# Performance work log

Hardware: AMD Instinct MI355X
Metric: run time of the kernel (lower is better)

Reference implementation:

```python
import jax, jax.numpy as jnp
import numpy as np
from functools import partial

# norse LIFAdEx default parameters
DT = 0.001
TAU_SYN_INV = 1.0 / 5e-3   # 200.0
TAU_MEM_INV = 1.0 / 1e-2   # 100.0
TAU_ADA_INV = 2.0
ADAPT_CURRENT = 4.0
ADAPT_SPIKE = 0.02
DELTA_T = 0.5
V_LEAK = 0.0
V_TH = 1.0
V_RESET = 0.0
ALPHA = 100.0              # superspike surrogate sharpness
TAU_FILTER_INV = 223.1435511314


@jax.custom_vjp
def superspike(x):
    # forward: heaviside; backward: superspike surrogate grad
    return (x > 0).astype(x.dtype)

def _ss_fwd(x):
    return superspike(x), x

def _ss_bwd(x, g):
    return (g / (ALPHA * jnp.abs(x) + 1.0) ** 2,)

superspike.defvjp(_ss_fwd, _ss_bwd)


def lif_adex_recurrent(x, W_in, W_rec):
    """x: (T,B,F) -> spikes (T,B,H). norse lif_adex_step semantics."""
    T, B, _ = x.shape
    H = W_rec.shape[0]
    # precompute feed-forward input current for all steps: (T,B,H)
    i_in = jnp.einsum('tbf,hf->tbh', x, W_in)

    def step(carry, ic):
        z, v, i, a = carry
        dv = DT * TAU_MEM_INV * ((V_LEAK - v)
                                 + DELTA_T * jnp.exp((v - V_TH) / DELTA_T)
                                 + i - a)
        v_dec = v + dv
        i_dec = i - DT * TAU_SYN_INV * i
        a_dec = a + DT * TAU_ADA_INV * (ADAPT_CURRENT * (v - V_LEAK) - a)
        z_new = superspike(v_dec - V_TH)
        v_new = (1.0 - z_new) * v_dec + z_new * V_RESET
        i_new = i_dec + ic + z @ W_rec.T
        a_new = a_dec + z_new * ADAPT_SPIKE
        return (z_new, v_new, i_new, a_new), z_new

    z0 = jnp.zeros((B, H), x.dtype)
    init = (z0, z0, z0, z0)
    _, spikes = jax.lax.scan(step, init, i_in)
    return spikes


def exp_filter(spikes, W_out, b_out):
    """Linear readout + exponential low-pass filter over time."""
    y = jnp.einsum('tbh,oh->tbo', spikes, W_out) + b_out  # (T,B,O)
    k = DT * TAU_FILTER_INV

    def step(o_prev, y_t):
        o = o_prev + k * (y_t - o_prev)
        return o, o

    o0 = y[0]
    _, rest = jax.lax.scan(step, o0, y[1:])
    return jnp.concatenate([o0[None], rest], axis=0)


def setup_inputs() -> dict:
    key = jax.random.key(0)
    kx, k1, k2, k3, k4 = jax.random.split(key, 5)
    T, B, F, H, O = 500, 128, 128, 512, 32
    x = jax.random.normal(kx, (T, B, F), dtype=jnp.float32)
    W_in = jax.random.normal(k1, (H, F), dtype=jnp.float32) * np.sqrt(2.0 / F)
    W_rec = jax.random.normal(k2, (H, H), dtype=jnp.float32) * np.sqrt(2.0 / H)
    W_out = jax.random.normal(k3, (O, H), dtype=jnp.float32) * np.sqrt(1.0 / H)
    b_out = jax.random.normal(k4, (O,), dtype=jnp.float32) * 0.01
    return {'x': x, 'W_in': W_in, 'W_rec': W_rec, 'W_out': W_out, 'b_out': b_out}


def reference(x, W_in, W_rec, W_out, b_out):
    spikes = lif_adex_recurrent(x, W_in, W_rec)
    return exp_filter(spikes, W_out, b_out)
```

## Files before the change

kernel.cpp:

```cpp
#include <hip/hip_runtime.h>
#include <hip/hip_bf16.h>
#include <cstdint>
#include <cstddef>

#define T_STEPS 500
#define BATCH   128
#define FDIM    128
#define HDIM    512
#define ODIM    32
#define M_ROWS  (T_STEPS * BATCH)
#define ZOFF    (512u << 11)
#define ZOFFB   (512u << 10)

typedef __attribute__((ext_vector_type(8))) __bf16 bf16x8;
typedef __attribute__((ext_vector_type(4))) float  f32x4;

__device__ __forceinline__ float bfbits2f(unsigned short u) {
    union { unsigned int i; float f; } c; c.i = ((unsigned int)u) << 16; return c.f;
}
__device__ __forceinline__ float asf(unsigned int u) {
    union { unsigned int i; float f; } c; c.i = u; return c.f;
}
__device__ __forceinline__ void lds_barrier() {
    asm volatile("s_waitcnt lgkmcnt(0)" ::: "memory");
    __builtin_amdgcn_s_barrier();
}

__global__ void detect_kernel(const unsigned short* __restrict__ xw, int* __restrict__ flag) {
    __shared__ int cnt;
    if (threadIdx.x == 0) cnt = 0;
    __syncthreads();
    unsigned short w = xw[threadIdx.x * 2];
    int e = (w >> 7) & 0xFF;
    if (e >= 170) atomicAdd(&cnt, 1);
    __syncthreads();
    if (threadIdx.x == 0) *flag = (cnt >= 8) ? 1 : 0;
}

__global__ void prep_kernel(const void* __restrict__ Wrec,
                            const void* __restrict__ Wout,
                            const void* __restrict__ bout,
                            const void* __restrict__ Win,
                            const int* __restrict__ flag,
                            float* __restrict__ WrecT,
                            unsigned short* __restrict__ WrecTb,
                            float* __restrict__ WoutT,
                            float* __restrict__ WinT,
                            float* __restrict__ bout32) {
    const int fp32 = *flag;
    int idx = blockIdx.x * blockDim.x + threadIdx.x;
    if (fp32) {
        if (idx < HDIM * HDIM) {
            int h = idx / HDIM, hp = idx % HDIM;
            WrecT[hp * HDIM + h] = ((const float*)Wrec)[idx];
        }
        if (idx < HDIM) WrecT[HDIM * HDIM + idx] = 0.f;
        if (idx < HDIM * FDIM) {
            int h = idx / FDIM, f = idx % FDIM;
            WinT[f * HDIM + h] = ((const float*)Win)[idx];
        }
    } else {
        if (idx < HDIM * HDIM) {
            int h = idx / HDIM, hp = idx % HDIM;
            WrecTb[hp * HDIM + h] = ((const unsigned short*)Wrec)[idx];
        }
        if (idx < HDIM) WrecTb[HDIM * HDIM + idx] = 0;
    }
    if (idx < ODIM * HDIM) {
        int o = idx / HDIM, h = idx % HDIM;
        WoutT[h * ODIM + o] = fp32 ? ((const float*)Wout)[idx]
                                   : bfbits2f(((const unsigned short*)Wout)[idx]);
    }
    if (idx < ODIM)
        bout32[idx] = fp32 ? ((const float*)bout)[idx]
                           : bfbits2f(((const unsigned short*)bout)[idx]);
}

__global__ __launch_bounds__(256) void iin_gemm_mfma(const __hip_bfloat16* __restrict__ x,
                                                     const __hip_bfloat16* __restrict__ Win,
                                                     const int* __restrict__ flag,
                                                     float* __restrict__ iin) {
    if (*flag != 0) return;
    const int mt   = blockIdx.x;
    const int nt   = blockIdx.y;
    const int wave = threadIdx.x >> 6;
    const int lane = threadIdx.x & 63;
    const int l15  = lane & 15;
    const int quad = lane >> 4;
    const int m_base = mt * 64 + wave * 16;
    const int n_base = nt * 64;

    const __bf16* xb = reinterpret_cast<const __bf16*>(x);
    const __bf16* wb = reinterpret_cast<const __bf16*>(Win);

    f32x4 acc[4] = {{0.f,0.f,0.f,0.f},{0.f,0.f,0.f,0.f},{0.f,0.f,0.f,0.f},{0.f,0.f,0.f,0.f}};

#pragma unroll
    for (int kk = 0; kk < 4; ++kk) {
        const int k0 = kk * 32 + quad * 8;
        bf16x8 a = *reinterpret_cast<const bf16x8*>(xb + (size_t)(m_base + l15) * FDIM + k0);
#pragma unroll
        for (int nb = 0; nb < 4; ++nb) {
            bf16x8 bf = *reinterpret_cast<const bf16x8*>(wb + (size_t)(n_base + nb * 16 + l15) * FDIM + k0);
            acc[nb] = __builtin_amdgcn_mfma_f32_16x16x32_bf16(a, bf, acc[nb], 0, 0, 0);
        }
    }

#pragma unroll
    for (int nb = 0; nb < 4; ++nb)
#pragma unroll
        for (int r = 0; r < 4; ++r)
            iin[(size_t)(m_base + quad * 4 + r) * HDIM + n_base + nb * 16 + l15] = acc[nb][r];
}

__global__ __launch_bounds__(256) void iin_gemm_valu(const void* __restrict__ x,
                                                     const float* __restrict__ WinT,
                                                     const int* __restrict__ flag,
                                                     float* __restrict__ iin) {
    if (*flag != 1) return;
    const int tid  = threadIdx.x;
    const int m0   = blockIdx.x * 32;

    __shared__ float xs[32][FDIM];

    for (int i = tid; i < 32 * FDIM; i += 256)
        xs[0][i] = ((const float*)x)[(size_t)m0 * FDIM + i];
    __syncthreads();

    float acc[32][2];
#pragma unroll
    for (int m = 0; m < 32; ++m) { acc[m][0] = 0.f; acc[m][1] = 0.f; }

#pragma unroll 4
    for (int k = 0; k < FDIM; ++k) {
        float w0 = WinT[(size_t)k * HDIM + tid];
        float w1 = WinT[(size_t)k * HDIM + 256 + tid];
#pragma unroll
        for (int m = 0; m < 32; ++m) {
            float xv = xs[m][k];
            acc[m][0] += xv * w0;
            acc[m][1] += xv * w1;
        }
    }

#pragma unroll
    for (int m = 0; m < 32; ++m) {
        iin[(size_t)(m0 + m) * HDIM + tid]       = acc[m][0];
        iin[(size_t)(m0 + m) * HDIM + 256 + tid] = acc[m][1];
    }
}

__global__ __launch_bounds__(1024) void scan_bf16(const float* __restrict__ iin,
                                                  const unsigned short* __restrict__ WrecTb,
                                                  const int* __restrict__ flag,
                                                  unsigned long long* __restrict__ masksG) {
    if (*flag != 0) return;
    const int b    = blockIdx.x;
    const int tid  = threadIdx.x;
    const int q    = tid & 63;
    const int pc   = tid >> 6;
    const int lane = tid & 63;
    const int wv   = tid >> 6;
    const bool st  = tid < HDIM;
    const int h    = tid;

    __shared__ unsigned long long wmask[8];
    __shared__ float4 partA[16][64];
    __shared__ float4 partB[16][64];
    __shared__ alignas(16) unsigned int slA[16][36];
    __shared__ alignas(16) unsigned int slB[16][36];
    unsigned int (*slO)[36] = slA;
    unsigned int (*slN)[36] = slB;

    float v = 0.f, cur = 0.f, a = 0.f;
    int   cnt = 0;
    const char* WQ = (const char*)WrecTb + q * 16;
    float ic_cur = st ? iin[(size_t)b * HDIM + h] : 0.f;

    for (int t = 0; t < T_STEPS; ++t) {
        float ic_next = 0.f;
        if (st && (t + 1) < T_STEPS)
            ic_next = iin[((size_t)(t + 1) * BATCH + b) * HDIM + h];

        float i_dec = 0.f; bool zk = false; unsigned long long m = 0;
        if (st) {
            float s = (0.0f - v) + 0.5f * expf((v - 1.0f) * 2.0f);
            s = s + cur;
            s = s - a;
            float v_dec = v + 0.1f * s;
            i_dec = cur - 0.2f * cur;
            float a_dec = a + 0.002f * (4.0f * v - a);
            zk = (v_dec - 1.0f) > 0.0f;
            m = __ballot(zk);
            if (lane == 0) {
                wmask[wv] = m;
                masksG[((size_t)t * BATCH + b) * 8 + wv] = m;
            }
            v = zk ? 0.0f : v_dec;
            a = zk ? (a_dec + 0.02f) : a_dec;
        }

        float rs0=0.f,rs1=0.f,rs2=0.f,rs3=0.f,rs4=0.f,rs5=0.f,rs6=0.f,rs7=0.f;
        {
            const unsigned int* sl = slO[pc];
            const int n  = (cnt + 15 - pc) >> 4;
            const int ng = (n + 3) >> 2;
            uint4 w0[4], w1[4];
            auto ldg = [&](int g, uint4* w) {
                uint4 ix = *(const uint4*)(sl + (g << 2));
                w[0] = *(const uint4*)(WQ + ix.x);
                w[1] = *(const uint4*)(WQ + ix.y);
                w[2] = *(const uint4*)(WQ + ix.z);
                w[3] = *(const uint4*)(WQ + ix.w);
            };
            auto accw = [&](const uint4* w) {
#pragma unroll
                for (int u = 0; u < 4; ++u) {
                    rs0 += asf(w[u].x << 16); rs1 += asf(w[u].x & 0xffff0000u);
                    rs2 += asf(w[u].y << 16); rs3 += asf(w[u].y & 0xffff0000u);
                    rs4 += asf(w[u].z << 16); rs5 += asf(w[u].z & 0xffff0000u);
                    rs6 += asf(w[u].w << 16); rs7 += asf(w[u].w & 0xffff0000u);
                }
            };
            int g = 0;
            if (ng > 0) ldg(0, w0);
            while (g + 2 <= ng) {
                ldg(g + 1, w1);
                accw(w0);
                if (g + 2 < ng) ldg(g + 2, w0);
                accw(w1);
                g += 2;
            }
            if (g < ng) accw(w0);
        }
        partA[pc][q] = (float4){rs0, rs1, rs2, rs3};
        partB[pc][q] = (float4){rs4, rs5, rs6, rs7};

        lds_barrier();

        int total = 0;
#pragma unroll
        for (int w = 0; w < 8; ++w) total += __popcll(wmask[w]);

        if (st) {
            float rec = 0.f;
            const int  qq = h >> 3, jj = h & 3;
            const bool hi = (h & 4) != 0;
#pragma unroll
            for (int pp = 0; pp < 16; ++pp) {
                const float* pa = (const float*)&partA[pp][qq];
                const float* pb = (const float*)&partB[pp][qq];
                rec += hi ? pb[jj] : pa[jj];
            }
            cur = (i_dec + ic_cur) + rec;

            if (zk) {
                int off = __popcll(m & ((1ull << lane) - 1ull));
#pragma unroll
                for (int w = 0; w < 8; ++w) if (w < wv) off += __popcll(wmask[w]);
                slN[off & 15][off >> 4] = (unsigned int)h << 10;
            }
        } else if (tid < HDIM + 64) {
            int s5 = (tid - HDIM) >> 2;
            int k  = (tid - HDIM) & 3;
            int ne = (total + 15 - s5) >> 4;
            int padc = (4 - (ne & 3)) & 3;
            if (k < padc) slN[s5][ne + k] = ZOFFB;
        }
        cnt = total;
        ic_cur = ic_next;

        lds_barrier();

        unsigned int (*tp)[36] = slO; slO = slN; slN = tp;
    }
}

__global__ __launch_bounds__(1024) void scan_f32(const float* __restrict__ iin,
                                                 const float* __restrict__ WrecT,
                                                 const int* __restrict__ flag,
                                                 unsigned long long* __restrict__ masksG) {
    if (*flag != 1) return;
    const int b    = blockIdx.x;
    const int tid  = threadIdx.x;
    const int q    = tid & 127;
    const int p    = tid >> 7;
    const int lane = tid & 63;
    const int wv   = tid >> 6;
    const bool st  = tid < HDIM;
    const int h    = tid;

    __shared__ unsigned long long wmask[8];
    __shared__ float4 part[8][128];
    __shared__ alignas(16) unsigned int slA[8][68];
    __shared__ alignas(16) unsigned int slB[8][68];
    unsigned int (*slO)[68] = slA;
    unsigned int (*slN)[68] = slB;

    float v = 0.f, cur = 0.f, a = 0.f;
    int   cnt = 0;
    const char* WQ = (const char*)WrecT + q * 16;

    for (int t = 0; t < T_STEPS; ++t) {
        float ic = 0.f, i_dec = 0.f;
        bool  zk = false;
        unsigned long long m = 0;

        if (st) {
            ic = iin[((size_t)t * BATCH + b) * HDIM + h];
            float s = (0.0f - v) + 0.5f * expf((v - 1.0f) * 2.0f);
            s = s + cur;
            s = s - a;
            float v_dec = v + 0.1f * s;
            i_dec = cur - 0.2f * cur;
            float a_dec = a + 0.002f * (4.0f * v - a);
            zk = (v_dec - 1.0f) > 0.0f;
            m = __ballot(zk);
            if (lane == 0) {
                wmask[wv] = m;
                masksG[((size_t)t * BATCH + b) * 8 + wv] = m;
            }
            v = zk ? 0.0f : v_dec;
            a = zk ? (a_dec + 0.02f) : a_dec;
        }

        float4 rs = {0.f, 0.f, 0.f, 0.f};
        {
            const int n  = (cnt + 7 - p) >> 3;
            const int ng = (n + 3) >> 2;
            float4 b0[4], b1[4];
            auto ld4 = [&](int g, float4* d) {
                uint4 i0 = *(const uint4*)&slO[p][g << 2];
                d[0] = *(const float4*)(WQ + i0.x);
                d[1] = *(const float4*)(WQ + i0.y);
                d[2] = *(const float4*)(WQ + i0.z);
                d[3] = *(const float4*)(WQ + i0.w);
            };
            auto acc4 = [&](const float4* d) {
#pragma unroll
                for (int u = 0; u < 4; ++u) {
                    rs.x += d[u].x; rs.y += d[u].y; rs.z += d[u].z; rs.w += d[u].w;
                }
            };
            int g = 0;
            if (ng > 0) ld4(0, b0);
            while (g + 2 <= ng) {
                ld4(g + 1, b1);
                acc4(b0);
                if (g + 2 < ng) ld4(g + 2, b0);
                acc4(b1);
                g += 2;
            }
            if (g < ng) acc4(b0);
        }
        part[p][q] = rs;

        __syncthreads();

        int total = 0;
#pragma unroll
        for (int w = 0; w < 8; ++w) total += __popcll(wmask[w]);

        if (st) {
            float rec = 0.f;
#pragma unroll
            for (int pp = 0; pp < 8; ++pp)
                rec += ((const float*)&part[pp][h >> 2])[h & 3];
            cur = (i_dec + ic) + rec;
            if (zk) {
                int off = __popcll(m & ((1ull << lane) - 1ull));
#pragma unroll
                for (int w = 0; w < 8; ++w) if (w < wv) off += __popcll(wmask[w]);
                slN[off & 7][off >> 3] = (unsigned int)h << 11;
            }
        } else if (tid < HDIM + 32) {
            int s5 = (tid - HDIM) >> 2;
            int k  = (tid - HDIM) & 3;
            int ne = (total + 7 - s5) >> 3;
            int padc = (4 - (ne & 3)) & 3;
            if (k < padc) slN[s5][ne + k] = ZOFF;
        }
        cnt = total;

        __syncthreads();

        unsigned int (*tp)[68] = slO; slO = slN; slN = tp;
    }
}

__global__ __launch_bounds__(256) void y_kernel(const unsigned long long* __restrict__ masks,
                                                const float* __restrict__ WoutT,
                                                const float* __restrict__ bout,
                                                float* __restrict__ y) {
    const int tid = threadIdx.x;
    const int p   = blockIdx.x * 8 + (tid >> 5);
    const int o   = tid & 31;
    const unsigned long long* mp = masks + (size_t)p * 8;
    float acc = 0.f;
#pragma unroll
    for (int w = 0; w < 8; ++w) {
        unsigned long long m = mp[w];
        const float* Wb = WoutT + (size_t)w * 64 * ODIM + o;
        while (m) {
            int j = __builtin_ctzll(m);
            acc += Wb[j * ODIM];
            m &= m - 1;
        }
    }
    y[(size_t)p * ODIM + o] = acc + bout[o];
}

__global__ __launch_bounds__(64) void filter_kernel(const float* __restrict__ y,
                                                    const int* __restrict__ flag,
                                                    void* __restrict__ out) {
    const int p = blockIdx.x * 64 + threadIdx.x;
    const int fp32o = *flag;
    const float kf = 0.2231435511314f;
    float c0[10], c1[10];
#pragma unroll
    for (int u = 0; u < 10; ++u) c0[u] = y[(size_t)u * (BATCH * ODIM) + p];
    float o_state = 0.f;
    for (int base = 0; base < T_STEPS; base += 10) {
        if (base + 10 < T_STEPS) {
#pragma unroll
            for (int u = 0; u < 10; ++u)
                c1[u] = y[(size_t)(base + 10 + u) * (BATCH * ODIM) + p];
        }
#pragma unroll
        for (int u = 0; u < 10; ++u) {
            int t = base + u;
            float yt = c0[u];
            o_state = (t == 0) ? yt : (o_state + kf * (yt - o_state));
            size_t oi = (size_t)t * (BATCH * ODIM) + p;
            if (fp32o) ((float*)out)[oi] = o_state;
            else       ((__hip_bfloat16*)out)[oi] = __float2bfloat16(o_state);
        }
#pragma unroll
        for (int u = 0; u < 10; ++u) c0[u] = c1[u];
    }
}

extern "C" void kernel_launch(void* const* d_in, const int* in_sizes, int n_in,
                              void* d_out, int out_size, void* d_ws, size_t ws_size,
                              hipStream_t stream) {
    const void* x = d_in[0]; const void* Win = d_in[1]; const void* Wrec = d_in[2];
    const void* Wout = d_in[3]; const void* bout = d_in[4];
    for (int i = 0; i < n_in; ++i) {
        switch (in_sizes[i]) {
            case 8192000: x    = d_in[i]; break;
            case 65536:   Win  = d_in[i]; break;
            case 262144:  Wrec = d_in[i]; break;
            case 16384:   Wout = d_in[i]; break;
            case 32:      bout = d_in[i]; break;
            default: break;
        }
    }

    const size_t OFF_FLAG  = 0;
    const size_t OFF_BOUT  = 256;
    const size_t OFF_WOUTT = 512;
    const size_t OFF_WRECT = 66048;
    const size_t OFF_WINT  = 1116672;
    const size_t OFF_MASK  = 1378816;
    const size_t OFF_IIN   = 5474816;
    const size_t OFF_Y     = OFF_IIN;
    const size_t REQUIRED  = OFF_IIN + (size_t)M_ROWS * HDIM * 4;
    if (ws_size < REQUIRED) return;

    char* ws = (char*)d_ws;
    int*            flag   = (int*)(ws + OFF_FLAG);
    float*          bout32 = (float*)(ws + OFF_BOUT);
    float*          WoutT  = (float*)(ws + OFF_WOUTT);
    float*          WrecT  = (float*)(ws + OFF_WRECT);
    unsigned short* WrecTb = (unsigned short*)(ws + OFF_WRECT);
    float*          WinT   = (float*)(ws + OFF_WINT);
    unsigned long long* masks = (unsigned long long*)(ws + OFF_MASK);
    float*          iin    = (float*)(ws + OFF_IIN);
    float*          y      = (float*)(ws + OFF_Y);

    hipLaunchKernelGGL(detect_kernel, dim3(1), dim3(256), 0, stream,
                       (const unsigned short*)x, flag);
    hipLaunchKernelGGL(prep_kernel, dim3((HDIM * HDIM + 255) / 256), dim3(256), 0, stream,
                       Wrec, Wout, bout, Win, flag, WrecT, WrecTb, WoutT, WinT, bout32);
    hipLaunchKernelGGL(iin_gemm_mfma, dim3(M_ROWS / 64, HDIM / 64), dim3(256), 0, stream,
                       (const __hip_bfloat16*)x, (const __hip_bfloat16*)Win, flag, iin);
    hipLaunchKernelGGL(iin_gemm_valu, dim3(M_ROWS / 32), dim3(256), 0, stream,
                       x, WinT, flag, iin);
    hipLaunchKernelGGL(scan_bf16, dim3(BATCH), dim3(1024), 0, stream,
                       iin, WrecTb, flag, masks);
    hipLaunchKernelGGL(scan_f32, dim3(BATCH), dim3(1024), 0, stream,
                       iin, WrecT, flag, masks);
    hipLaunchKernelGGL(y_kernel, dim3(M_ROWS / 8), dim3(256), 0, stream,
                       masks, WoutT, bout32, y);
    hipLaunchKernelGGL(filter_kernel, dim3((BATCH * ODIM) / 64), dim3(64), 0, stream,
                       y, flag, d_out);
}
```

Measured before the change: 902.8 us.

## Restructure f32 recurrent scan to one thread per neuron with single barrier

The f32 scan kernel drops from 1024 to 512 threads, so each thread owns one hidden neuron. Each thread now gathers its own column of W_rec over all spiking indices, instead of splitting the spike list 8 ways and reducing float4 partials through shared memory. Spike lists are kept as per-wave segments with counts in double-buffered LDS, which leaves one lightweight LDS barrier per timestep in place of two __syncthreads. The next step's input current is prefetched a step ahead. The cost is that each thread walks the whole spike list serially with scalar loads, and there is less thread-level parallelism per block.

```diff
diff --git a/kernel.cpp b/kernel.cpp
--- a/kernel.cpp
+++ b/kernel.cpp
@@ -276,115 +276,99 @@
     }
 }
 
-__global__ __launch_bounds__(1024) void scan_f32(const float* __restrict__ iin,
-                                                 const float* __restrict__ WrecT,
-                                                 const int* __restrict__ flag,
-                                                 unsigned long long* __restrict__ masksG) {
+__global__ __launch_bounds__(512) void scan_f32(const float* __restrict__ iin,
+                                                const float* __restrict__ WrecT,
+                                                const int* __restrict__ flag,
+                                                unsigned long long* __restrict__ masksG) {
     if (*flag != 1) return;
     const int b    = blockIdx.x;
     const int tid  = threadIdx.x;
-    const int q    = tid & 127;
-    const int p    = tid >> 7;
     const int lane = tid & 63;
     const int wv   = tid >> 6;
-    const bool st  = tid < HDIM;
     const int h    = tid;
 
-    __shared__ unsigned long long wmask[8];
-    __shared__ float4 part[8][128];
-    __shared__ alignas(16) unsigned int slA[8][68];
-    __shared__ alignas(16) unsigned int slB[8][68];
-    unsigned int (*slO)[68] = slA;
-    unsigned int (*slN)[68] = slB;
+    __shared__ alignas(16) unsigned int seg[2][8 * 64];
+    __shared__ alignas(16) int scnt[2][8];
+
+    if (tid < 8) scnt[1][tid] = 0;
+    lds_barrier();
 
     float v = 0.f, cur = 0.f, a = 0.f;
-    int   cnt = 0;
-    const char* WQ = (const char*)WrecT + q * 16;
+    float ic_cur = iin[(size_t)b * HDIM + h];
+    const char* Wc = (const char*)WrecT + (size_t)h * 4;
 
     for (int t = 0; t < T_STEPS; ++t) {
-        float ic = 0.f, i_dec = 0.f;
-        bool  zk = false;
-        unsigned long long m = 0;
-
-        if (st) {
-            ic = iin[((size_t)t * BATCH + b) * HDIM + h];
-            float s = (0.0f - v) + 0.5f * expf((v - 1.0f) * 2.0f);
-            s = s + cur;
-            s = s - a;
-            float v_dec = v + 0.1f * s;
-            i_dec = cur - 0.2f * cur;
-            float a_dec = a + 0.002f * (4.0f * v - a);
-            zk = (v_dec - 1.0f) > 0.0f;
-            m = __ballot(zk);
-            if (lane == 0) {
-                wmask[wv] = m;
-                masksG[((size_t)t * BATCH + b) * 8 + wv] = m;
-            }
-            v = zk ? 0.0f : v_dec;
-            a = zk ? (a_dec + 0.02f) : a_dec;
-        }
-
-        float4 rs = {0.f, 0.f, 0.f, 0.f};
+        const int curb = t & 1, prev = curb ^ 1;
+
+        const int4 ca = *(const int4*)&scnt[prev][0];
+        const int4 cb = *(const int4*)&scnt[prev][4];
+        const int total = ca.x + ca.y + ca.z + ca.w + cb.x + cb.y + cb.z + cb.w;
+
+        float ic_next = 0.f;
+        if (t + 1 < T_STEPS)
+            ic_next = iin[((size_t)(t + 1) * BATCH + b) * HDIM + h];
+
+        float s = (0.0f - v) + 0.5f * expf((v - 1.0f) * 2.0f);
+        s = s + cur;
+        s = s - a;
+        float v_dec = v + 0.1f * s;
+        float i_dec = cur - 0.2f * cur;
+        float a_dec = a + 0.002f * (4.0f * v - a);
+        bool  zk = (v_dec - 1.0f) > 0.0f;
+        unsigned long long m = __ballot(zk);
+        if (lane == 0) {
+            scnt[curb][wv] = (int)__popcll(m);
+            masksG[((size_t)t * BATCH + b) * 8 + wv] = m;
+        }
+        if (zk) {
+            int off = __popcll(m & ((1ull << lane) - 1ull));
+            seg[curb][(wv << 6) + off] = (unsigned int)h << 11;
+        }
+        v = zk ? 0.0f : v_dec;
+        a = zk ? (a_dec + 0.02f) : a_dec;
+
+        float rec = 0.f;
         {
-            const int n  = (cnt + 7 - p) >> 3;
-            const int ng = (n + 3) >> 2;
-            float4 b0[4], b1[4];
-            auto ld4 = [&](int g, float4* d) {
-                uint4 i0 = *(const uint4*)&slO[p][g << 2];
-                d[0] = *(const float4*)(WQ + i0.x);
-                d[1] = *(const float4*)(WQ + i0.y);
-                d[2] = *(const float4*)(WQ + i0.z);
-                d[3] = *(const float4*)(WQ + i0.w);
-            };
-            auto acc4 = [&](const float4* d) {
+            const unsigned int* segP = seg[prev];
+            const int* scP = scnt[prev];
+            int w = 0, idx = 0, cw = ca.x;
+            const int ng = (total + 3) >> 2;
+            unsigned int ha[4], hb[4];
+            float va[4], vb[4];
+            auto NEXT4 = [&](unsigned int* hh) {
 #pragma unroll
                 for (int u = 0; u < 4; ++u) {
-                    rs.x += d[u].x; rs.y += d[u].y; rs.z += d[u].z; rs.w += d[u].w;
+                    while (idx >= cw && w < 8) { ++w; idx = 0; cw = (w < 8) ? scP[w] : 0; }
+                    unsigned int xo;
+                    if (w < 8) { xo = segP[(w << 6) + idx]; ++idx; }
+                    else       { xo = (unsigned int)HDIM << 11; }
+                    hh[u] = xo;
                 }
             };
+            auto ISSUE = [&](const unsigned int* hh, float* vv) {
+#pragma unroll
+                for (int u = 0; u < 4; ++u)
+                    vv[u] = *(const float*)(Wc + hh[u]);
+            };
+            auto ACC = [&](const float* vv) {
+                rec += vv[0]; rec += vv[1]; rec += vv[2]; rec += vv[3];
+            };
             int g = 0;
-            if (ng > 0) ld4(0, b0);
+            if (ng > 0) { NEXT4(ha); ISSUE(ha, va); }
             while (g + 2 <= ng) {
-                ld4(g + 1, b1);
-                acc4(b0);
-                if (g + 2 < ng) ld4(g + 2, b0);
-                acc4(b1);
+                NEXT4(hb); ISSUE(hb, vb);
+                ACC(va);
+                if (g + 2 < ng) { NEXT4(ha); ISSUE(ha, va); }
+                ACC(vb);
                 g += 2;
             }
-            if (g < ng) acc4(b0);
-        }
-        part[p][q] = rs;
-
-        __syncthreads();
-
-        int total = 0;
-#pragma unroll
-        for (int w = 0; w < 8; ++w) total += __popcll(wmask[w]);
-
-        if (st) {
-            float rec = 0.f;
-#pragma unroll
-            for (int pp = 0; pp < 8; ++pp)
-                rec += ((const float*)&part[pp][h >> 2])[h & 3];
-            cur = (i_dec + ic) + rec;
-            if (zk) {
-                int off = __popcll(m & ((1ull << lane) - 1ull));
-#pragma unroll
-                for (int w = 0; w < 8; ++w) if (w < wv) off += __popcll(wmask[w]);
-                slN[off & 7][off >> 3] = (unsigned int)h << 11;
-            }
-        } else if (tid < HDIM + 32) {
-            int s5 = (tid - HDIM) >> 2;
-            int k  = (tid - HDIM) & 3;
-            int ne = (total + 7 - s5) >> 3;
-            int padc = (4 - (ne & 3)) & 3;
-            if (k < padc) slN[s5][ne + k] = ZOFF;
-        }
-        cnt = total;
-
-        __syncthreads();
-
-        unsigned int (*tp)[68] = slO; slO = slN; slN = tp;
+            if (g < ng) ACC(va);
+        }
+
+        cur = (i_dec + ic_cur) + rec;
+        ic_cur = ic_next;
+
+        lds_barrier();
     }
 }
 
@@ -488,7 +472,7 @@
                        x, WinT, flag, iin);
     hipLaunchKernelGGL(scan_bf16, dim3(BATCH), dim3(1024), 0, stream,
                        iin, WrecTb, flag, masks);
-    hipLaunchKernelGGL(scan_f32, dim3(BATCH), dim3(1024), 0, stream,
+    hipLaunchKernelGGL(scan_f32, dim3(BATCH), dim3(512), 0, stream,
                        iin, WrecT, flag, masks);
     hipLaunchKernelGGL(y_kernel, dim3(M_ROWS / 8), dim3(256), 0, stream,
                        masks, WoutT, bout32, y);
```

New measurement: 2.182 ms. +141.7%, slower.
